# Optimization experiments

Measured on AMD Instinct MI355X. Metric: run time of the kernel, lower is better.

The kernel has to match this reference:

```python
import jax, jax.numpy as jnp
import numpy as np

EPS_LN = 1e-5
EPS_COS = 1e-8
EPS_AREA = 5e-4


def _ln(x, g, b):
    m = jnp.mean(x, axis=-1, keepdims=True)
    v = jnp.mean((x - m) ** 2, axis=-1, keepdims=True)
    return (x - m) / jnp.sqrt(v + EPS_LN) * g + b


def _wgap(f, m):
    # f: (b, N, c), m: (b, N) -> (b, c); matches masked avg_pool2d trick
    num = jnp.einsum('bnc,bn->bc', f, m)
    den = jnp.sum(m, axis=1, keepdims=True) + EPS_AREA
    return num / den


def _cos_tok(k, p):
    # k: (b, N, c) tokens vs p: (b, c) prototype, cosine over channel dim
    dot = jnp.einsum('bnc,bc->bn', k, p)
    nk = jnp.linalg.norm(k, axis=-1)
    np_ = jnp.linalg.norm(p, axis=-1, keepdims=True)
    return dot / (jnp.maximum(nk, EPS_COS) * jnp.maximum(np_, EPS_COS))


def _cos_vec(a, b):
    # a, b: (b, c) -> (b,)
    dot = jnp.sum(a * b, axis=-1)
    na = jnp.linalg.norm(a, axis=-1)
    nb = jnp.linalg.norm(b, axis=-1)
    return dot / (jnp.maximum(na, EPS_COS) * jnp.maximum(nb, EPS_COS))


def _mlp(x, W1, b1, W2, b2):
    h = jax.nn.gelu(x @ W1.T + b1, approximate=False)
    return h @ W2.T + b2


def setup_inputs() -> dict:
    key = jax.random.key(0)
    ks = jax.random.split(key, 32)
    b, H, W, c = 8, 64, 64, 512
    N = H * W
    hid = 4 * c
    s = 0.02
    inp = {
        'x': jax.random.normal(ks[0], (b, N, c), jnp.float32),
        'y': jax.random.normal(ks[1], (b, N, c), jnp.float32),
        'mask': (jax.random.uniform(ks[2], (b, N)) > 0.5).astype(jnp.float32),
        'pro_pred': jax.random.uniform(ks[3], (b, 1, H, W), jnp.float32),
        'g1': jnp.ones((c,), jnp.float32), 'beta1': jnp.zeros((c,), jnp.float32),
        'g2': jnp.ones((c,), jnp.float32), 'beta2': jnp.zeros((c,), jnp.float32),
        'Wq': jax.random.normal(ks[4], (c, c)) * s,
        'Wk': jax.random.normal(ks[5], (c, c)) * s,
        'Wv': jax.random.normal(ks[6], (c, c)) * s,
        'Wx1': jax.random.normal(ks[7], (c, 2 * c)) * s,
        'Wx2': jax.random.normal(ks[8], (c, 2 * c)) * s,
        'Wfx': jax.random.normal(ks[9], (c, 2 * c)) * s,
        'Wy1': jax.random.normal(ks[10], (c, 2 * c)) * s,
        'Wy2': jax.random.normal(ks[11], (c, 2 * c)) * s,
        'Wfy': jax.random.normal(ks[12], (c, 2 * c)) * s,
        'W1x': jax.random.normal(ks[13], (hid, c)) * s, 'b1x': jnp.zeros((hid,)),
        'W2x': jax.random.normal(ks[14], (c, hid)) * s, 'b2x': jnp.zeros((c,)),
        'W1y': jax.random.normal(ks[15], (hid, c)) * s, 'b1y': jnp.zeros((hid,)),
        'W2y': jax.random.normal(ks[16], (c, hid)) * s, 'b2y': jnp.zeros((c,)),
        'h': 64, 'w': 64,
    }
    return inp


def reference(x, y, mask, pro_pred, g1, beta1, g2, beta2, Wq, Wk, Wv,
              Wx1, Wx2, Wfx, Wy1, Wy2, Wfy,
              W1x, b1x, W2x, b2x, W1y, b1y, W2y, b2y, h, w):
    b, N, c = x.shape
    x_skip, y_skip = x, y
    xn = _ln(x, g1, beta1)
    yn = _ln(y, g1, beta1)
    q = yn @ Wq.T            # support features (b, N, c)
    k = xn @ Wk.T            # query features
    v = xn @ Wv.T

    m = mask                 # (b, N)
    fg_pro = _wgap(q, m)             # (b, c)
    bg_pro = _wgap(q, 1.0 - m)

    sim_fg = _cos_tok(k, fg_pro) * 10.0   # (b, N)
    sim_bg = _cos_tok(k, bg_pro) * 10.0
    logits = jnp.stack([sim_bg, sim_fg], axis=1)     # (b, 2, N)
    pseudo = jax.nn.softmax(logits, axis=1)

    query_fg1 = _wgap(v, pseudo[:, 1, :])            # (b, c)
    s1 = (_cos_vec(query_fg1, fg_pro)[:, None] + 1.0) / 2.0
    pro1 = s1 * fg_pro + (1.0 - s1) * query_fg1      # (b, c)

    query_fg2 = _wgap(v, pro_pred.reshape(b, N))
    s2 = (_cos_vec(query_fg2, fg_pro)[:, None] + 1.0) / 2.0
    pro2 = s2 * fg_pro + (1.0 - s2) * query_fg2

    p1 = jnp.broadcast_to(pro1[:, None, :], (b, N, c))
    p2 = jnp.broadcast_to(pro2[:, None, :], (b, N, c))

    x1 = jnp.concatenate([x_skip, p1], axis=-1) @ Wx1.T
    x2 = jnp.concatenate([x_skip, p2], axis=-1) @ Wx2.T
    x_merge = jnp.concatenate([x1, x2], axis=-1) @ Wfx.T + x_skip

    y1 = jnp.concatenate([y_skip, p1], axis=-1) @ Wy1.T
    y2 = jnp.concatenate([y_skip, p2], axis=-1) @ Wy2.T
    y_merge = jnp.concatenate([y1, y2], axis=-1) @ Wfy.T + y_skip

    x_out = x + _mlp(_ln(x_merge, g2, beta2), W1x, b1x, W2x, b2x)
    y_out = y + _mlp(_ln(y_merge, g2, beta2), W1y, b1y, W2y, b2y)
    pseudo_mask = pseudo.reshape(b, 2, h, w)
    return x_out, y_out, pseudo_mask
```

## Files before the change

kernel.cpp:

```cpp
#include <hip/hip_runtime.h>
#include <stdint.h>

typedef unsigned short u16;
typedef unsigned int   u32;

typedef __attribute__((ext_vector_type(8))) __bf16 bf16x8;
typedef __attribute__((ext_vector_type(4))) float  f32x4;

#define GLD_LDS(g, l) __builtin_amdgcn_global_load_lds( \
    (__attribute__((address_space(1))) void*)(g),        \
    (__attribute__((address_space(3))) void*)(l), 16, 0, 0)

__device__ __forceinline__ float bf2f(u16 h) {
    union { u32 u; float f; } c; c.u = ((u32)h) << 16; return c.f;
}
__device__ __forceinline__ u16 f2bf(float f) {
    union { float f; u32 u; } c; c.f = f;
    return (u16)((c.u + 0x7FFFu + ((c.u >> 16) & 1u)) >> 16);
}
__device__ __forceinline__ u32 pack2(float a, float b) {
    return (u32)f2bf(a) | ((u32)f2bf(b) << 16);
}
__device__ __forceinline__ uint4 pack8(float4 a, float4 b) {
    return make_uint4(pack2(a.x, a.y), pack2(a.z, a.w), pack2(b.x, b.y), pack2(b.z, b.w));
}
__device__ __forceinline__ void unpack8(uint4 u, float v[8]) {
    v[0] = bf2f((u16)(u.x & 0xffff)); v[1] = bf2f((u16)(u.x >> 16));
    v[2] = bf2f((u16)(u.y & 0xffff)); v[3] = bf2f((u16)(u.y >> 16));
    v[4] = bf2f((u16)(u.z & 0xffff)); v[5] = bf2f((u16)(u.z >> 16));
    v[6] = bf2f((u16)(u.w & 0xffff)); v[7] = bf2f((u16)(u.w >> 16));
}
__device__ __forceinline__ float wsum(float v) {
#pragma unroll
    for (int o = 32; o > 0; o >>= 1) v += __shfl_xor(v, o, 64);
    return v;
}
__device__ __forceinline__ float fast_gelu(float x) {
    const float u = x * (1.f + 0.044715f * x * x);
    return x / (1.f + __expf(-1.5957691216f * u));
}

__global__ __launch_bounds__(256)
void cvt4_kernel(const float* __restrict__ a, const float* __restrict__ b,
                 const float* __restrict__ c, const float* __restrict__ d,
                 u16* __restrict__ oa, u16* __restrict__ ob,
                 u16* __restrict__ oc, u16* __restrict__ od, int n8)
{
    const int i = blockIdx.x * 256 + threadIdx.x;
    if (i >= n8) return;
    const int z = blockIdx.y;
    const float* in = (z == 0) ? a : (z == 1) ? b : (z == 2) ? c : d;
    u16* out = (z == 0) ? oa : (z == 1) ? ob : (z == 2) ? oc : od;
    const float* p = in + (size_t)i * 8;
    float4 u = *(const float4*)p, v = *(const float4*)(p + 4);
    *(uint4*)(out + (size_t)i * 8) = pack8(u, v);
}
__global__ __launch_bounds__(256)
void cvt3_kernel(const float* __restrict__ a, const float* __restrict__ b,
                 const float* __restrict__ c,
                 u16* __restrict__ oa, u16* __restrict__ ob, u16* __restrict__ oc, int n8)
{
    const int i = blockIdx.x * 256 + threadIdx.x;
    if (i >= n8) return;
    const int z = blockIdx.y;
    const float* in = (z == 0) ? a : (z == 1) ? b : c;
    u16* out = (z == 0) ? oa : (z == 1) ? ob : oc;
    const float* p = in + (size_t)i * 8;
    float4 u = *(const float4*)p, v = *(const float4*)(p + 4);
    *(uint4*)(out + (size_t)i * 8) = pack8(u, v);
}

template<bool IN16, bool RAW>
__device__ __forceinline__ void ln_body(const void* in, u16* out,
                                        const float* g, const float* be, u16* raw_out)
{
    const int lane = threadIdx.x & 63;
    const size_t row = (size_t)blockIdx.x * 4 + (threadIdx.x >> 6);
    const size_t base = row * 512 + lane * 8;
    float v[8];
    if constexpr (IN16) {
        unpack8(*(const uint4*)((const u16*)in + base), v);
    } else {
        const float* p = (const float*)in + base;
        float4 a = *(const float4*)p, b = *(const float4*)(p + 4);
        v[0]=a.x; v[1]=a.y; v[2]=a.z; v[3]=a.w; v[4]=b.x; v[5]=b.y; v[6]=b.z; v[7]=b.w;
    }
    if constexpr (RAW) {
        u32 ro[4];
#pragma unroll
        for (int i = 0; i < 4; ++i) ro[i] = pack2(v[2*i], v[2*i+1]);
        *(uint4*)(raw_out + base) = make_uint4(ro[0], ro[1], ro[2], ro[3]);
    }
    float s = 0.f, ss = 0.f;
#pragma unroll
    for (int i = 0; i < 8; ++i) { s += v[i]; ss += v[i] * v[i]; }
    s = wsum(s); ss = wsum(ss);
    const float mean = s * (1.f / 512.f);
    const float rstd = rsqrtf(ss * (1.f / 512.f) - mean * mean + 1e-5f);
    const float* gp = g + lane * 8;
    const float* bp = be + lane * 8;
    u32 o[4];
#pragma unroll
    for (int i = 0; i < 4; ++i) {
        u16 lo = f2bf((v[2*i]   - mean) * rstd * gp[2*i]   + bp[2*i]);
        u16 hi = f2bf((v[2*i+1] - mean) * rstd * gp[2*i+1] + bp[2*i+1]);
        o[i] = (u32)lo | ((u32)hi << 16);
    }
    *(uint4*)(out + base) = make_uint4(o[0], o[1], o[2], o[3]);
}

template<bool IN16, bool RAW>
__global__ __launch_bounds__(256)
void ln_kernel(const void* __restrict__ in, u16* __restrict__ out,
               const float* __restrict__ g, const float* __restrict__ be,
               u16* __restrict__ raw_out)
{
    ln_body<IN16, RAW>(in, out, g, be, raw_out);
}

template<bool IN16, bool RAW>
__global__ __launch_bounds__(256)
void ln2_kernel(const void* __restrict__ in0, u16* __restrict__ out0, u16* __restrict__ raw0,
                const void* __restrict__ in1, u16* __restrict__ out1, u16* __restrict__ raw1,
                const float* __restrict__ g, const float* __restrict__ be)
{
    if (blockIdx.y == 0) ln_body<IN16, RAW>(in0, out0, g, be, raw0);
    else                 ln_body<IN16, RAW>(in1, out1, g, be, raw1);
}

template<bool IS16>
__device__ __forceinline__ void load_pair(const void* P, size_t off, size_t rstep,
                                          uint4& r0, uint4& r1)
{
    if constexpr (IS16) {
        const u16* p = (const u16*)P + off;
        r0 = *(const uint4*)p;
        r1 = *(const uint4*)(p + rstep);
    } else {
        const float* p = (const float*)P + off;
        float4 a0 = *(const float4*)p,           a1 = *(const float4*)(p + 4);
        float4 b0 = *(const float4*)(p + rstep), b1 = *(const float4*)(p + rstep + 4);
        r0 = pack8(a0, a1);
        r1 = pack8(b0, b1);
    }
}

template<int EPI, bool OUT16>
__global__ __launch_bounds__(512)
void gemm3_kernel(const u16* __restrict__ A, const u16* __restrict__ B,
                  void* __restrict__ Cp, int N, int K,
                  const float* __restrict__ bias_b,
                  const float* __restrict__ bias_v,
                  const float* __restrict__ skip)
{
    __shared__ u16 sA[2][128 * 32];
    __shared__ u16 sB[2][256 * 32];
    const int t = threadIdx.x;
    const int w = t >> 6;
    const int lane = t & 63;
    const int lr = lane & 15;
    const int lk = lane >> 4;
    const int bm0 = blockIdx.x * 128;
    const int bn0 = blockIdx.y * 256;
    const int wrow = (w >> 2) * 64;
    const int wcol = (w & 3) * 64;

    f32x4 acc[4][4];
#pragma unroll
    for (int m = 0; m < 4; ++m)
#pragma unroll
        for (int n = 0; n < 4; ++n) acc[m][n] = (f32x4){0.f, 0.f, 0.f, 0.f};

    const int scol = ((t & 3) ^ ((t >> 3) & 3)) * 8;
    const u16* gA = A + (size_t)(bm0 + (t >> 2)) * K + scol;
    const u16* gB = B + (size_t)(bn0 + (t >> 2)) * K + scol;
    const size_t rstep = (size_t)128 * K;
    const int wo = w << 9;
    const int sa = (lk ^ ((lr >> 1) & 3)) * 8;

    GLD_LDS(gA, sA[0] + wo);
    GLD_LDS(gB, sB[0] + wo);
    GLD_LDS(gB + rstep, sB[0] + 4096 + wo);
    __syncthreads();

    int cur = 0;
    for (int kt = 32; kt <= K; kt += 32) {
        if (kt < K) {
            const int nxt = cur ^ 1;
            GLD_LDS(gA + kt, sA[nxt] + wo);
            GLD_LDS(gB + kt, sB[nxt] + wo);
            GLD_LDS(gB + kt + rstep, sB[nxt] + 4096 + wo);
        }
        bf16x8 af[4], bfr[4];
#pragma unroll
        for (int m = 0; m < 4; ++m)
            af[m] = *(const bf16x8*)&sA[cur][(wrow + m * 16 + lr) * 32 + sa];
#pragma unroll
        for (int n = 0; n < 4; ++n)
            bfr[n] = *(const bf16x8*)&sB[cur][(wcol + n * 16 + lr) * 32 + sa];
#pragma unroll
        for (int m = 0; m < 4; ++m)
#pragma unroll
            for (int n = 0; n < 4; ++n)
                acc[m][n] = __builtin_amdgcn_mfma_f32_16x16x32_bf16(af[m], bfr[n], acc[m][n], 0, 0, 0);
        if (kt < K) { __syncthreads(); cur ^= 1; }
    }

#pragma unroll
    for (int m = 0; m < 4; ++m) {
#pragma unroll
        for (int n = 0; n < 4; ++n) {
            const int col = bn0 + wcol + n * 16 + lr;
#pragma unroll
            for (int r = 0; r < 4; ++r) {
                const int row = bm0 + wrow + m * 16 + lk * 4 + r;
                const size_t idx = (size_t)row * N + col;
                float vv = acc[m][n][r];
                if (EPI == 1) vv += bias_b[(size_t)(row >> 12) * N + col] + skip[idx];
                if (EPI == 2) { vv += bias_v[col]; vv = fast_gelu(vv); }
                if (EPI == 3) vv += bias_v[col] + skip[idx];
                if (OUT16) ((u16*)Cp)[idx] = f2bf(vv);
                else       ((float*)Cp)[idx] = vv;
            }
        }
    }
}

template<int EPI, bool OUT16>
__global__ __launch_bounds__(256)
void gemm2_kernel(const u16* __restrict__ A, const u16* __restrict__ B,
                  void* __restrict__ Cp, int N, int K,
                  const float* __restrict__ bias_b,
                  const float* __restrict__ bias_v,
                  const float* __restrict__ skip)
{
    __shared__ u16 sA[2][128 * 32];
    __shared__ u16 sB[2][128 * 32];
    const int t = threadIdx.x;
    const int w = t >> 6;
    const int lane = t & 63;
    const int lr = lane & 15;
    const int lk = lane >> 4;
    const int bm0 = blockIdx.x * 128;
    const int bn0 = blockIdx.y * 128;
    const int wrow = (w >> 1) * 64;
    const int wcol = (w & 1) * 64;

    f32x4 acc[4][4];
#pragma unroll
    for (int m = 0; m < 4; ++m)
#pragma unroll
        for (int n = 0; n < 4; ++n) acc[m][n] = (f32x4){0.f, 0.f, 0.f, 0.f};

    const int scol = ((t & 3) ^ ((t >> 3) & 3)) * 8;
    const u16* gA = A + (size_t)(bm0 + (t >> 2)) * K + scol;
    const u16* gB = B + (size_t)(bn0 + (t >> 2)) * K + scol;
    const size_t rstep = (size_t)64 * K;
    const int wo = w << 9;
    const int sa = (lk ^ ((lr >> 1) & 3)) * 8;

    GLD_LDS(gA, sA[0] + wo); GLD_LDS(gA + rstep, sA[0] + wo + 2048);
    GLD_LDS(gB, sB[0] + wo); GLD_LDS(gB + rstep, sB[0] + wo + 2048);
    __syncthreads();

    int cur = 0;
    for (int kt = 32; kt <= K; kt += 32) {
        if (kt < K) {
            const int nxt = cur ^ 1;
            GLD_LDS(gA + kt, sA[nxt] + wo); GLD_LDS(gA + kt + rstep, sA[nxt] + wo + 2048);
            GLD_LDS(gB + kt, sB[nxt] + wo); GLD_LDS(gB + kt + rstep, sB[nxt] + wo + 2048);
        }
        bf16x8 af[4], bfr[4];
#pragma unroll
        for (int m = 0; m < 4; ++m)
            af[m] = *(const bf16x8*)&sA[cur][(wrow + m * 16 + lr) * 32 + sa];
#pragma unroll
        for (int n = 0; n < 4; ++n)
            bfr[n] = *(const bf16x8*)&sB[cur][(wcol + n * 16 + lr) * 32 + sa];
#pragma unroll
        for (int m = 0; m < 4; ++m)
#pragma unroll
            for (int n = 0; n < 4; ++n)
                acc[m][n] = __builtin_amdgcn_mfma_f32_16x16x32_bf16(af[m], bfr[n], acc[m][n], 0, 0, 0);
        if (kt < K) { __syncthreads(); cur ^= 1; }
    }

#pragma unroll
    for (int m = 0; m < 4; ++m) {
#pragma unroll
        for (int n = 0; n < 4; ++n) {
            const int col = bn0 + wcol + n * 16 + lr;
#pragma unroll
            for (int r = 0; r < 4; ++r) {
                const int row = bm0 + wrow + m * 16 + lk * 4 + r;
                const size_t idx = (size_t)row * N + col;
                float vv = acc[m][n][r];
                if (EPI == 1) vv += bias_b[(size_t)(row >> 12) * N + col] + skip[idx];
                if (EPI == 2) { vv += bias_v[col]; vv = fast_gelu(vv); }
                if (EPI == 3) vv += bias_v[col] + skip[idx];
                if (OUT16) ((u16*)Cp)[idx] = f2bf(vv);
                else       ((float*)Cp)[idx] = vv;
            }
        }
    }
}

template<int WM>
__global__ __launch_bounds__(512)
void gemm3_red_kernel(const u16* __restrict__ A, const u16* __restrict__ B, int K,
                      const float* __restrict__ wa, const float* __restrict__ wb,
                      float* __restrict__ acc1, float* __restrict__ acc2)
{
    __shared__ u16 sA[2][128 * 32];
    __shared__ u16 sB[2][256 * 32];
    __shared__ float sred[8][2][64];
    const int t = threadIdx.x;
    const int w = t >> 6;
    const int lane = t & 63;
    const int lr = lane & 15;
    const int lk = lane >> 4;
    const int bm0 = blockIdx.x * 128;
    const int bn0 = blockIdx.y * 256;
    const int wrow = (w >> 2) * 64;
    const int wcol = (w & 3) * 64;

    f32x4 acc[4][4];
#pragma unroll
    for (int m = 0; m < 4; ++m)
#pragma unroll
        for (int n = 0; n < 4; ++n) acc[m][n] = (f32x4){0.f, 0.f, 0.f, 0.f};

    const int scol = ((t & 3) ^ ((t >> 3) & 3)) * 8;
    const u16* gA = A + (size_t)(bm0 + (t >> 2)) * K + scol;
    const u16* gB = B + (size_t)(bn0 + (t >> 2)) * K + scol;
    const size_t rstep = (size_t)128 * K;
    const int wo = w << 9;
    const int sa = (lk ^ ((lr >> 1) & 3)) * 8;

    GLD_LDS(gA, sA[0] + wo);
    GLD_LDS(gB, sB[0] + wo);
    GLD_LDS(gB + rstep, sB[0] + 4096 + wo);
    __syncthreads();

    int cur = 0;
    for (int kt = 32; kt <= K; kt += 32) {
        if (kt < K) {
            const int nxt = cur ^ 1;
            GLD_LDS(gA + kt, sA[nxt] + wo);
            GLD_LDS(gB + kt, sB[nxt] + wo);
            GLD_LDS(gB + kt + rstep, sB[nxt] + 4096 + wo);
        }
        bf16x8 af[4], bfr[4];
#pragma unroll
        for (int m = 0; m < 4; ++m)
            af[m] = *(const bf16x8*)&sA[cur][(wrow + m * 16 + lr) * 32 + sa];
#pragma unroll
        for (int n = 0; n < 4; ++n)
            bfr[n] = *(const bf16x8*)&sB[cur][(wcol + n * 16 + lr) * 32 + sa];
#pragma unroll
        for (int m = 0; m < 4; ++m)
#pragma unroll
            for (int n = 0; n < 4; ++n)
                acc[m][n] = __builtin_amdgcn_mfma_f32_16x16x32_bf16(af[m], bfr[n], acc[m][n], 0, 0, 0);
        if (kt < K) { __syncthreads(); cur ^= 1; }
    }

    float w1v[16], w2v[16];
#pragma unroll
    for (int m = 0; m < 4; ++m)
#pragma unroll
        for (int r = 0; r < 4; ++r) {
            const int row = bm0 + wrow + m * 16 + lk * 4 + r;
            if (WM == 0) { float mm = wa[row]; w1v[m*4+r] = mm; w2v[m*4+r] = 1.f - mm; }
            else         { w1v[m*4+r] = wa[row]; w2v[m*4+r] = wb[row]; }
        }
    __syncthreads();
#pragma unroll
    for (int n = 0; n < 4; ++n) {
        float s1 = 0.f, s2 = 0.f;
#pragma unroll
        for (int m = 0; m < 4; ++m)
#pragma unroll
            for (int r = 0; r < 4; ++r) {
                s1 += acc[m][n][r] * w1v[m*4+r];
                s2 += acc[m][n][r] * w2v[m*4+r];
            }
        s1 += __shfl_xor(s1, 16, 64); s1 += __shfl_xor(s1, 32, 64);
        s2 += __shfl_xor(s2, 16, 64); s2 += __shfl_xor(s2, 32, 64);
        if (lk == 0) { sred[w][0][n*16+lr] = s1; sred[w][1][n*16+lr] = s2; }
    }
    __syncthreads();
    if (t < 256) {
        const int strip = t >> 6, c = t & 63;
        const float v1 = sred[strip][0][c] + sred[strip + 4][0][c];
        const float v2 = sred[strip][1][c] + sred[strip + 4][1][c];
        const int col = bn0 + strip * 64 + c;
        const int b = bm0 >> 12;
        atomicAdd(&acc1[b * 512 + col], v1);
        atomicAdd(&acc2[b * 512 + col], v2);
    }
}

template<int EPI, bool A16, bool B16, bool OUT16>
__global__ __launch_bounds__(256)
void gemm_kernel(const void* __restrict__ Ap, const void* __restrict__ Wp,
                 void* __restrict__ Cp, int N, int K,
                 const float* __restrict__ bias_b,
                 const float* __restrict__ bias_v,
                 const float* __restrict__ skip)
{
    __shared__ u16 sA[128 * 32];
    __shared__ u16 sB[128 * 32];
    const int t = threadIdx.x;
    const int w = t >> 6;
    const int lane = t & 63;
    const int lr = lane & 15;
    const int lk = lane >> 4;
    const int bm0 = blockIdx.x * 128;
    const int bn0 = blockIdx.y * 128;
    const int wrow = (w >> 1) * 64;
    const int wcol = (w & 1) * 64;

    f32x4 acc[4][4];
#pragma unroll
    for (int m = 0; m < 4; ++m)
#pragma unroll
        for (int n = 0; n < 4; ++n) acc[m][n] = (f32x4){0.f, 0.f, 0.f, 0.f};

    const size_t aoff = (size_t)(bm0 + (t >> 2)) * K + (t & 3) * 8;
    const size_t boff = (size_t)(bn0 + (t >> 2)) * K + (t & 3) * 8;
    const size_t rstep = (size_t)64 * K;
    u16* dA = sA + 8 * t;
    u16* dB = sB + 8 * t;

    for (int kt = 0; kt < K; kt += 32) {
        uint4 ra0, ra1, rb0, rb1;
        load_pair<A16>(Ap, aoff + kt, rstep, ra0, ra1);
        load_pair<B16>(Wp, boff + kt, rstep, rb0, rb1);
        __syncthreads();
        *(uint4*)dA = ra0; *(uint4*)(dA + 2048) = ra1;
        *(uint4*)dB = rb0; *(uint4*)(dB + 2048) = rb1;
        __syncthreads();
        bf16x8 af[4], bfr[4];
#pragma unroll
        for (int m = 0; m < 4; ++m)
            af[m] = *(const bf16x8*)&sA[(wrow + m * 16 + lr) * 32 + lk * 8];
#pragma unroll
        for (int n = 0; n < 4; ++n)
            bfr[n] = *(const bf16x8*)&sB[(wcol + n * 16 + lr) * 32 + lk * 8];
#pragma unroll
        for (int m = 0; m < 4; ++m)
#pragma unroll
            for (int n = 0; n < 4; ++n)
                acc[m][n] = __builtin_amdgcn_mfma_f32_16x16x32_bf16(af[m], bfr[n], acc[m][n], 0, 0, 0);
    }

#pragma unroll
    for (int m = 0; m < 4; ++m) {
#pragma unroll
        for (int n = 0; n < 4; ++n) {
            const int col = bn0 + wcol + n * 16 + lr;
#pragma unroll
            for (int r = 0; r < 4; ++r) {
                const int row = bm0 + wrow + m * 16 + lk * 4 + r;
                const size_t idx = (size_t)row * N + col;
                float vv = acc[m][n][r];
                if (EPI == 1) vv += bias_b[(size_t)(row >> 12) * N + col] + skip[idx];
                if (EPI == 2) { vv += bias_v[col]; vv = fast_gelu(vv); }
                if (EPI == 3) vv += bias_v[col] + skip[idx];
                if (OUT16) ((u16*)Cp)[idx] = f2bf(vv);
                else       ((float*)Cp)[idx] = vv;
            }
        }
    }
}

template<int WM>
__global__ __launch_bounds__(256)
void gemm_red_kernel(const u16* __restrict__ A, const float* __restrict__ W, int K,
                     const float* __restrict__ wa, const float* __restrict__ wb,
                     float* __restrict__ acc1, float* __restrict__ acc2)
{
    __shared__ u16 sA[128 * 32];
    __shared__ u16 sB[128 * 32];
    __shared__ float sred[4][2][64];
    const int t = threadIdx.x;
    const int w = t >> 6;
    const int lane = t & 63;
    const int lr = lane & 15;
    const int lk = lane >> 4;
    const int bm0 = blockIdx.x * 128;
    const int bn0 = blockIdx.y * 128;
    const int wrow = (w >> 1) * 64;
    const int wcol = (w & 1) * 64;

    f32x4 acc[4][4];
#pragma unroll
    for (int m = 0; m < 4; ++m)
#pragma unroll
        for (int n = 0; n < 4; ++n) acc[m][n] = (f32x4){0.f, 0.f, 0.f, 0.f};

    const size_t aoff = (size_t)(bm0 + (t >> 2)) * K + (t & 3) * 8;
    const size_t boff = (size_t)(bn0 + (t >> 2)) * K + (t & 3) * 8;
    const size_t rstep = (size_t)64 * K;
    u16* dA = sA + 8 * t;
    u16* dB = sB + 8 * t;

    for (int kt = 0; kt < K; kt += 32) {
        uint4 ra0, ra1, rb0, rb1;
        load_pair<true >(A, aoff + kt, rstep, ra0, ra1);
        load_pair<false>(W, boff + kt, rstep, rb0, rb1);
        __syncthreads();
        *(uint4*)dA = ra0; *(uint4*)(dA + 2048) = ra1;
        *(uint4*)dB = rb0; *(uint4*)(dB + 2048) = rb1;
        __syncthreads();
        bf16x8 af[4], bfr[4];
#pragma unroll
        for (int m = 0; m < 4; ++m)
            af[m] = *(const bf16x8*)&sA[(wrow + m * 16 + lr) * 32 + lk * 8];
#pragma unroll
        for (int n = 0; n < 4; ++n)
            bfr[n] = *(const bf16x8*)&sB[(wcol + n * 16 + lr) * 32 + lk * 8];
#pragma unroll
        for (int m = 0; m < 4; ++m)
#pragma unroll
            for (int n = 0; n < 4; ++n)
                acc[m][n] = __builtin_amdgcn_mfma_f32_16x16x32_bf16(af[m], bfr[n], acc[m][n], 0, 0, 0);
    }

    float w1v[16], w2v[16];
#pragma unroll
    for (int m = 0; m < 4; ++m)
#pragma unroll
        for (int r = 0; r < 4; ++r) {
            const int row = bm0 + wrow + m * 16 + lk * 4 + r;
            if (WM == 0) { float mm = wa[row]; w1v[m*4+r] = mm; w2v[m*4+r] = 1.f - mm; }
            else         { w1v[m*4+r] = wa[row]; w2v[m*4+r] = wb[row]; }
        }
#pragma unroll
    for (int n = 0; n < 4; ++n) {
        float s1 = 0.f, s2 = 0.f;
#pragma unroll
        for (int m = 0; m < 4; ++m)
#pragma unroll
            for (int r = 0; r < 4; ++r) {
                s1 += acc[m][n][r] * w1v[m*4+r];
                s2 += acc[m][n][r] * w2v[m*4+r];
            }
        s1 += __shfl_xor(s1, 16, 64); s1 += __shfl_xor(s1, 32, 64);
        s2 += __shfl_xor(s2, 16, 64); s2 += __shfl_xor(s2, 32, 64);
        if (lk == 0) { sred[w][0][n*16+lr] = s1; sred[w][1][n*16+lr] = s2; }
    }
    __syncthreads();
// ... 119 lines not shown
                    const float* __restrict__ Wfy, const float* __restrict__ Wy1,
                    const float* __restrict__ Wy2, u16* __restrict__ My)
{
    const float* Wf = blockIdx.z ? Wfy : Wfx;
    const float* W1 = blockIdx.z ? Wy1 : Wx1;
    const float* W2 = blockIdx.z ? Wy2 : Wx2;
    u16* Mout = blockIdx.z ? My : Mx;
    const int i = blockIdx.x * 16 + threadIdx.x;
    const int o = blockIdx.y * 16 + threadIdx.y;
    float s = 0.f;
    for (int j = 0; j < 512; ++j) {
        s += Wf[o * 1024 + j]       * W1[j * 1024 + i];
        s += Wf[o * 1024 + 512 + j] * W2[j * 1024 + i];
    }
    Mout[o * 512 + i] = f2bf(s);
}

__global__ __launch_bounds__(512)
void tvec4_kernel(const float* __restrict__ Wx1, const float* __restrict__ Wx2,
                  const float* __restrict__ Wy1, const float* __restrict__ Wy2,
                  const float* __restrict__ pro1, const float* __restrict__ pro2,
                  float* __restrict__ t1x, float* __restrict__ t2x,
                  float* __restrict__ t1y, float* __restrict__ t2y)
{
    const int z = blockIdx.z;
    const float* W = (z == 0) ? Wx1 : (z == 1) ? Wx2 : (z == 2) ? Wy1 : Wy2;
    const float* p = (z & 1) ? pro2 : pro1;
    float* tout = (z == 0) ? t1x : (z == 1) ? t2x : (z == 2) ? t1y : t2y;
    const int lane = threadIdx.x & 63;
    const int j = blockIdx.x * 8 + (threadIdx.x >> 6);
    const int b = blockIdx.y;
    const float* wr = W + (size_t)j * 1024 + 512 + lane * 8;
    const float* pr = p + b * 512 + lane * 8;
    float4 w0 = *(const float4*)wr, w1 = *(const float4*)(wr + 4);
    float4 p0 = *(const float4*)pr, p1 = *(const float4*)(pr + 4);
    float s = w0.x*p0.x + w0.y*p0.y + w0.z*p0.z + w0.w*p0.w
            + w1.x*p1.x + w1.y*p1.y + w1.z*p1.z + w1.w*p1.w;
    s = wsum(s);
    if (lane == 0) tout[b * 512 + j] = s;
}

__global__ __launch_bounds__(512)
void biascomb2_kernel(const float* __restrict__ Wfx, const float* __restrict__ Wfy,
                      const float* __restrict__ t1x, const float* __restrict__ t2x,
                      const float* __restrict__ t1y, const float* __restrict__ t2y,
                      float* __restrict__ bias_x, float* __restrict__ bias_y)
{
    const int z = blockIdx.z;
    const float* Wf = z ? Wfy : Wfx;
    const float* t1 = z ? t1y : t1x;
    const float* t2 = z ? t2y : t2x;
    float* bias = z ? bias_y : bias_x;
    const int lane = threadIdx.x & 63;
    const int o = blockIdx.x * 8 + (threadIdx.x >> 6);
    const int b = blockIdx.y;
    const float* w1 = Wf + (size_t)o * 1024 + lane * 8;
    const float* tp1 = t1 + b * 512 + lane * 8;
    const float* tp2 = t2 + b * 512 + lane * 8;
    float s = 0.f;
#pragma unroll
    for (int h = 0; h < 2; ++h) {
        const float* wv = w1 + h * 512;
        const float* tp = h ? tp2 : tp1;
        float4 a0 = *(const float4*)wv, a1 = *(const float4*)(wv + 4);
        float4 b0 = *(const float4*)tp, b1 = *(const float4*)(tp + 4);
        s += a0.x*b0.x + a0.y*b0.y + a0.z*b0.z + a0.w*b0.w
           + a1.x*b1.x + a1.y*b1.y + a1.z*b1.z + a1.w*b1.w;
    }
    s = wsum(s);
    if (lane == 0) bias[b * 512 + o] = s;
}

extern "C" void kernel_launch(void* const* d_in, const int* in_sizes, int n_in,
                              void* d_out, int out_size, void* d_ws, size_t ws_size,
                              hipStream_t stream)
{
    const float* x   = (const float*)d_in[0];
    const float* y   = (const float*)d_in[1];
    const float* mask= (const float*)d_in[2];
    const float* pp  = (const float*)d_in[3];
    const float* g1  = (const float*)d_in[4];
    const float* be1 = (const float*)d_in[5];
    const float* g2  = (const float*)d_in[6];
    const float* be2 = (const float*)d_in[7];
    const float* Wq  = (const float*)d_in[8];
    const float* Wk  = (const float*)d_in[9];
    const float* Wv  = (const float*)d_in[10];
    const float* Wx1 = (const float*)d_in[11];
    const float* Wx2 = (const float*)d_in[12];
    const float* Wfx = (const float*)d_in[13];
    const float* Wy1 = (const float*)d_in[14];
    const float* Wy2 = (const float*)d_in[15];
    const float* Wfy = (const float*)d_in[16];
    const float* W1x = (const float*)d_in[17];
    const float* b1x = (const float*)d_in[18];
    const float* W2x = (const float*)d_in[19];
    const float* b2x = (const float*)d_in[20];
    const float* W1y = (const float*)d_in[21];
    const float* b1y = (const float*)d_in[22];
    const float* W2y = (const float*)d_in[23];
    const float* b2y = (const float*)d_in[24];

    if (ws_size < 69206016u) return;
    const bool fast = ws_size >= 78643200u;
    const bool huge = ws_size >= 145752064u;

    float* outx = (float*)d_out;
    float* outy = outx + 16777216;
    float* pmf  = outx + 33554432;

    char* wsb = (char*)d_ws;
    float* fsm = (float*)wsb;
    float* fgacc  = fsm;
    float* bgacc  = fsm + 4096;
    float* q1acc  = fsm + 8192;
    float* q2acc  = fsm + 12288;
    float* denq1  = fsm + 16384;
    float* denfg  = fsm + 16392;
    float* denq2  = fsm + 16400;
    float* nfg    = fsm + 16408;
    float* nbg    = fsm + 16416;
    float* fg_pro = fsm + 16424;
    float* bg_pro = fsm + 20520;
    float* pro1   = fsm + 24616;
    float* pro2   = fsm + 28712;
    float* t1x    = fsm + 32808;
    float* t2x    = fsm + 36904;
    float* t1y    = fsm + 41000;
    float* t2y    = fsm + 45096;
    float* bias_x = fsm + 49192;
    float* bias_y = fsm + 53288;
    float* pseudo = fsm + 57384;

    hipMemsetAsync(fsm, 0, 65568, stream);

    if (fast) {
        u16* Mx   = (u16*)(wsb + 0x60000);
        u16* My   = (u16*)(wsb + 0xE0000);
        u16* Wqb  = (u16*)(wsb + 0x160000);
        u16* Wkb  = (u16*)(wsb + 0x1E0000);
        u16* Wvb  = (u16*)(wsb + 0x260000);
        u16* W1xb = (u16*)(wsb + 0x2E0000);
        u16* W2xb = (u16*)(wsb + 0x4E0000);
        u16* W1yb = (u16*)(wsb + 0x6E0000);
        u16* W2yb = (u16*)(wsb + 0x8E0000);
        u16* WS0  = (u16*)(wsb + 0xB00000);
        u16* WS1  = WS0 + 16777216;
        u16* WS2  = WS1 + 16777216;

        u16* OX0 = (u16*)outx;
        u16* OX1 = OX0 + 16777216;
        u16* OY  = (u16*)outy;

        cvt3_kernel<<<dim3(128, 3), 256, 0, stream>>>(Wq, Wk, Wv, Wqb, Wkb, Wvb, 32768);
        cvt4_kernel<<<dim3(512, 4), 256, 0, stream>>>(W1x, W2x, W1y, W2y, W1xb, W2xb, W1yb, W2yb, 131072);
        mmcomb2_kernel<<<dim3(32, 32, 2), dim3(16, 16), 0, stream>>>(Wfx, Wx1, Wx2, Mx, Wfy, Wy1, Wy2, My);

        ln2_kernel<false, true><<<dim3(8192, 2), 256, 0, stream>>>(x, WS0, OX0, y, WS1, OY, g1, be1);

        dim3 gq(256, 2);
        gemm3_red_kernel<0><<<gq, 512, 0, stream>>>(WS1, Wqb, 512, mask, nullptr, fgacc, bgacc);
        rowsum2_kernel<<<dim3(8, 2), 256, 0, stream>>>(mask, denfg, pp, denq2);
        proto_fin_kernel<<<8, 512, 0, stream>>>(fgacc, bgacc, denfg, fg_pro, bg_pro, nfg, nbg);

        gemm3_kernel<0, true><<<gq, 512, 0, stream>>>(WS0, Wkb, OX1, 512, 512, nullptr, nullptr, nullptr);
        sim_kernel<<<8192, 256, 0, stream>>>(OX1, fg_pro, bg_pro, nfg, nbg, pseudo, pmf);
        rowsum_kernel<<<8, 256, 0, stream>>>(pseudo, denq1);

        gemm3_red_kernel<1><<<gq, 512, 0, stream>>>(WS0, Wvb, 512, pseudo, pp, q1acc, q2acc);
        proto2_kernel<<<8, 512, 0, stream>>>(q1acc, q2acc, denq1, denq2, fg_pro, nfg, pro1, pro2);

        tvec4_kernel<<<dim3(64, 8, 4), 512, 0, stream>>>(Wx1, Wx2, Wy1, Wy2, pro1, pro2, t1x, t2x, t1y, t2y);
        biascomb2_kernel<<<dim3(64, 8, 2), 512, 0, stream>>>(Wfx, Wfy, t1x, t2x, t1y, t2y, bias_x, bias_y);

        gemm3_kernel<1, true><<<gq, 512, 0, stream>>>(OX0, Mx, WS0, 512, 512, bias_x, nullptr, x);
        ln_kernel<true, false><<<8192, 256, 0, stream>>>(WS0, WS1, g2, be2, nullptr);
        gemm3_kernel<1, true><<<gq, 512, 0, stream>>>(OY, My, WS0, 512, 512, bias_y, nullptr, y);
        ln_kernel<true, false><<<8192, 256, 0, stream>>>(WS0, WS0, g2, be2, nullptr);

        for (int ch = 0; ch < 2; ++ch) {
            const size_t ro = (size_t)ch * 16384 * 512;
            gemm3_kernel<2, true><<<dim3(128, 8), 512, 0, stream>>>(WS1 + ro, W1xb, OY, 2048, 512, nullptr, b1x, nullptr);
            gemm2_kernel<3, false><<<dim3(128, 4), 256, 0, stream>>>(OY, W2xb, outx + ro, 512, 2048, nullptr, b2x, x + ro);
        }

        if (huge) {
            for (int ch = 0; ch < 2; ++ch) {
                const size_t ro = (size_t)ch * 16384 * 512;
                gemm3_kernel<2, true><<<dim3(128, 8), 512, 0, stream>>>(WS0 + ro, W1yb, WS2, 2048, 512, nullptr, b1y, nullptr);
                gemm2_kernel<3, false><<<dim3(128, 4), 256, 0, stream>>>(WS2, W2yb, outy + ro, 512, 2048, nullptr, b2y, y + ro);
            }
        } else {
            for (int ch = 0; ch < 4; ++ch) {
                const size_t ro = (size_t)ch * 8192 * 512;
                gemm3_kernel<2, true><<<dim3(64, 8), 512, 0, stream>>>(WS0 + ro, W1yb, WS1, 2048, 512, nullptr, b1y, nullptr);
                gemm2_kernel<3, false><<<dim3(64, 4), 256, 0, stream>>>(WS1, W2yb, outy + ro, 512, 2048, nullptr, b2y, y + ro);
            }
        }
    } else {
        u16* Mx  = (u16*)(wsb + 360608);
        u16* My  = (u16*)(wsb + 884896);
        u16* WS0 = (u16*)(wsb + 2097152);
        u16* WS1 = (u16*)(wsb + 35651584);

        ln_kernel<false, false><<<8192, 256, 0, stream>>>(x, WS0, g1, be1, nullptr);
        ln_kernel<false, false><<<8192, 256, 0, stream>>>(y, WS1, g1, be1, nullptr);

        dim3 g512(256, 4);
        gemm_red_kernel<0><<<g512, 256, 0, stream>>>(WS1, Wq, 512, mask, nullptr, fgacc, bgacc);
        rowsum_kernel<<<8, 256, 0, stream>>>(mask, denfg);
        rowsum_kernel<<<8, 256, 0, stream>>>(pp, denq2);
        proto_fin_kernel<<<8, 512, 0, stream>>>(fgacc, bgacc, denfg, fg_pro, bg_pro, nfg, nbg);

        gemm_kernel<0, true, false, true><<<g512, 256, 0, stream>>>(WS0, Wk, WS1, 512, 512, nullptr, nullptr, nullptr);
        sim_kernel<<<8192, 256, 0, stream>>>(WS1, fg_pro, bg_pro, nfg, nbg, pseudo, pmf);
        rowsum_kernel<<<8, 256, 0, stream>>>(pseudo, denq1);

        gemm_red_kernel<1><<<g512, 256, 0, stream>>>(WS0, Wv, 512, pseudo, pp, q1acc, q2acc);
        proto2_kernel<<<8, 512, 0, stream>>>(q1acc, q2acc, denq1, denq2, fg_pro, nfg, pro1, pro2);

        mmcomb2_kernel<<<dim3(32, 32, 2), dim3(16, 16), 0, stream>>>(Wfx, Wx1, Wx2, Mx, Wfy, Wy1, Wy2, My);
        tvec4_kernel<<<dim3(64, 8, 4), 512, 0, stream>>>(Wx1, Wx2, Wy1, Wy2, pro1, pro2, t1x, t2x, t1y, t2y);
        biascomb2_kernel<<<dim3(64, 8, 2), 512, 0, stream>>>(Wfx, Wfy, t1x, t2x, t1y, t2y, bias_x, bias_y);

        gemm_kernel<1, false, true, true><<<g512, 256, 0, stream>>>(x, Mx, WS0, 512, 512, bias_x, nullptr, x);
        ln_kernel<true, false><<<8192, 256, 0, stream>>>(WS0, WS1, g2, be2, nullptr);
        for (int ch = 0; ch < 4; ++ch) {
            const size_t ro = (size_t)ch * 8192 * 512;
            gemm_kernel<2, true, false, true><<<dim3(64, 16), 256, 0, stream>>>(WS1 + ro, W1x, WS0, 2048, 512, nullptr, b1x, nullptr);
            gemm_kernel<3, true, false, false><<<dim3(64, 4), 256, 0, stream>>>(WS0, W2x, outx + ro, 512, 2048, nullptr, b2x, x + ro);
        }
        gemm_kernel<1, false, true, true><<<g512, 256, 0, stream>>>(y, My, WS0, 512, 512, bias_y, nullptr, y);
        ln_kernel<true, false><<<8192, 256, 0, stream>>>(WS0, WS1, g2, be2, nullptr);
        for (int ch = 0; ch < 4; ++ch) {
            const size_t ro = (size_t)ch * 8192 * 512;
            gemm_kernel<2, true, false, true><<<dim3(64, 16), 256, 0, stream>>>(WS1 + ro, W1y, WS0, 2048, 512, nullptr, b1y, nullptr);
            gemm_kernel<3, true, false, false><<<dim3(64, 4), 256, 0, stream>>>(WS0, W2y, outy + ro, 512, 2048, nullptr, b2y, y + ro);
        }
    }
    (void)in_sizes; (void)n_in; (void)out_size;
}
```

Measured before the change: 871.4 us.

## Batch independent GEMMs into z-indexed launches and compute weight combos with MFMA

Refactors the GEMM kernels into device bodies so that independent GEMMs (the Q-reduction with the K projection, and the x/y merge GEMMs) run as a single launch using blockIdx.z. The per-stream fused merge weight product is now computed by converting and transposing the weights to bf16 and running the MFMA gemm2 path, replacing the previous mmcomb2 kernel. This cuts launch count and gives each launch a larger grid to fill the GPU. In exchange the combined weight matrix is computed in bf16 rather than fp32, and extra conversion and transpose kernels are added.

```diff
diff --git a/kernel.cpp b/kernel.cpp
--- a/kernel.cpp
+++ b/kernel.cpp
@@ -68,6 +68,37 @@
     const float* p = in + (size_t)i * 8;
     float4 u = *(const float4*)p, v = *(const float4*)(p + 4);
     *(uint4*)(out + (size_t)i * 8) = pack8(u, v);
+}
+__global__ __launch_bounds__(256)
+void cvt2_kernel(const float* __restrict__ a, const float* __restrict__ b,
+                 u16* __restrict__ oa, u16* __restrict__ ob, int n8)
+{
+    const int i = blockIdx.x * 256 + threadIdx.x;
+    if (i >= n8) return;
+    const float* in = blockIdx.y ? b : a;
+    u16* out = blockIdx.y ? ob : oa;
+    const float* p = in + (size_t)i * 8;
+    float4 u = *(const float4*)p, v = *(const float4*)(p + 4);
+    *(uint4*)(out + (size_t)i * 8) = pack8(u, v);
+}
+
+__global__ __launch_bounds__(256)
+void wtrans_kernel(const float* __restrict__ W1x, const float* __restrict__ W2x,
+                   const float* __restrict__ W1y, const float* __restrict__ W2y,
+                   u16* __restrict__ Wtx, u16* __restrict__ Wty)
+{
+    __shared__ float tile[32][33];
+    const int z = blockIdx.z;
+    const float* src = (z == 0) ? W1x : (z == 1) ? W2x : (z == 2) ? W1y : W2y;
+    u16* dst = (z < 2) ? Wtx : Wty;
+    const int joff = (z & 1) * 512;
+    const int j0 = blockIdx.y * 32;
+    const int i0 = blockIdx.x * 32;
+    for (int r = threadIdx.y; r < 32; r += 8)
+        tile[r][threadIdx.x] = src[(size_t)(j0 + r) * 1024 + i0 + threadIdx.x];
+    __syncthreads();
+    for (int r = threadIdx.y; r < 32; r += 8)
+        dst[(size_t)(i0 + r) * 1024 + joff + j0 + threadIdx.x] = f2bf(tile[threadIdx.x][r]);
 }
 
 template<bool IN16, bool RAW>
@@ -146,15 +177,10 @@
 }
 
 template<int EPI, bool OUT16>
-__global__ __launch_bounds__(512)
-void gemm3_kernel(const u16* __restrict__ A, const u16* __restrict__ B,
-                  void* __restrict__ Cp, int N, int K,
-                  const float* __restrict__ bias_b,
-                  const float* __restrict__ bias_v,
-                  const float* __restrict__ skip)
-{
-    __shared__ u16 sA[2][128 * 32];
-    __shared__ u16 sB[2][256 * 32];
+__device__ __forceinline__ void gemm3_body(const u16* A, const u16* B, void* Cp, int N, int K,
+                                           const float* bias_b, const float* bias_v, const float* skip,
+                                           u16 sA[2][128 * 32], u16 sB[2][256 * 32])
+{
     const int t = threadIdx.x;
     const int w = t >> 6;
     const int lane = t & 63;
@@ -226,16 +252,159 @@
     }
 }
 
+template<int WM>
+__device__ __forceinline__ void gemm3red_body(const u16* A, const u16* B, int K,
+                                              const float* wa, const float* wb,
+                                              float* acc1, float* acc2,
+                                              u16 sA[2][128 * 32], u16 sB[2][256 * 32],
+                                              float sred[8][2][64])
+{
+    const int t = threadIdx.x;
+    const int w = t >> 6;
+    const int lane = t & 63;
+    const int lr = lane & 15;
+    const int lk = lane >> 4;
+    const int bm0 = blockIdx.x * 128;
+    const int bn0 = blockIdx.y * 256;
+    const int wrow = (w >> 2) * 64;
+    const int wcol = (w & 3) * 64;
+
+    f32x4 acc[4][4];
+#pragma unroll
+    for (int m = 0; m < 4; ++m)
+#pragma unroll
+        for (int n = 0; n < 4; ++n) acc[m][n] = (f32x4){0.f, 0.f, 0.f, 0.f};
+
+    const int scol = ((t & 3) ^ ((t >> 3) & 3)) * 8;
+    const u16* gA = A + (size_t)(bm0 + (t >> 2)) * K + scol;
+    const u16* gB = B + (size_t)(bn0 + (t >> 2)) * K + scol;
+    const size_t rstep = (size_t)128 * K;
+    const int wo = w << 9;
+    const int sa = (lk ^ ((lr >> 1) & 3)) * 8;
+
+    GLD_LDS(gA, sA[0] + wo);
+    GLD_LDS(gB, sB[0] + wo);
+    GLD_LDS(gB + rstep, sB[0] + 4096 + wo);
+    __syncthreads();
+
+    int cur = 0;
+    for (int kt = 32; kt <= K; kt += 32) {
+        if (kt < K) {
+            const int nxt = cur ^ 1;
+            GLD_LDS(gA + kt, sA[nxt] + wo);
+            GLD_LDS(gB + kt, sB[nxt] + wo);
+            GLD_LDS(gB + kt + rstep, sB[nxt] + 4096 + wo);
+        }
+        bf16x8 af[4], bfr[4];
+#pragma unroll
+        for (int m = 0; m < 4; ++m)
+            af[m] = *(const bf16x8*)&sA[cur][(wrow + m * 16 + lr) * 32 + sa];
+#pragma unroll
+        for (int n = 0; n < 4; ++n)
+            bfr[n] = *(const bf16x8*)&sB[cur][(wcol + n * 16 + lr) * 32 + sa];
+#pragma unroll
+        for (int m = 0; m < 4; ++m)
+#pragma unroll
+            for (int n = 0; n < 4; ++n)
+                acc[m][n] = __builtin_amdgcn_mfma_f32_16x16x32_bf16(af[m], bfr[n], acc[m][n], 0, 0, 0);
+        if (kt < K) { __syncthreads(); cur ^= 1; }
+    }
+
+    float w1v[16], w2v[16];
+#pragma unroll
+    for (int m = 0; m < 4; ++m)
+#pragma unroll
+        for (int r = 0; r < 4; ++r) {
+            const int row = bm0 + wrow + m * 16 + lk * 4 + r;
+            if (WM == 0) { float mm = wa[row]; w1v[m*4+r] = mm; w2v[m*4+r] = 1.f - mm; }
+            else         { w1v[m*4+r] = wa[row]; w2v[m*4+r] = wb[row]; }
+        }
+    __syncthreads();
+#pragma unroll
+    for (int n = 0; n < 4; ++n) {
+        float s1 = 0.f, s2 = 0.f;
+#pragma unroll
+        for (int m = 0; m < 4; ++m)
+#pragma unroll
+            for (int r = 0; r < 4; ++r) {
+                s1 += acc[m][n][r] * w1v[m*4+r];
+                s2 += acc[m][n][r] * w2v[m*4+r];
+            }
+        s1 += __shfl_xor(s1, 16, 64); s1 += __shfl_xor(s1, 32, 64);
+        s2 += __shfl_xor(s2, 16, 64); s2 += __shfl_xor(s2, 32, 64);
+        if (lk == 0) { sred[w][0][n*16+lr] = s1; sred[w][1][n*16+lr] = s2; }
+    }
+    __syncthreads();
+    if (t < 256) {
+        const int strip = t >> 6, c = t & 63;
+        const float v1 = sred[strip][0][c] + sred[strip + 4][0][c];
+        const float v2 = sred[strip][1][c] + sred[strip + 4][1][c];
+        const int col = bn0 + strip * 64 + c;
+        const int b = bm0 >> 12;
+        atomicAdd(&acc1[b * 512 + col], v1);
+        atomicAdd(&acc2[b * 512 + col], v2);
+    }
+}
+
 template<int EPI, bool OUT16>
-__global__ __launch_bounds__(256)
-void gemm2_kernel(const u16* __restrict__ A, const u16* __restrict__ B,
+__global__ __launch_bounds__(512)
+void gemm3_kernel(const u16* __restrict__ A, const u16* __restrict__ B,
                   void* __restrict__ Cp, int N, int K,
                   const float* __restrict__ bias_b,
                   const float* __restrict__ bias_v,
                   const float* __restrict__ skip)
 {
     __shared__ u16 sA[2][128 * 32];
-    __shared__ u16 sB[2][128 * 32];
+    __shared__ u16 sB[2][256 * 32];
+    gemm3_body<EPI, OUT16>(A, B, Cp, N, K, bias_b, bias_v, skip, sA, sB);
+}
+
+template<int WM>
+__global__ __launch_bounds__(512)
+void gemm3_red_kernel(const u16* __restrict__ A, const u16* __restrict__ B, int K,
+                      const float* __restrict__ wa, const float* __restrict__ wb,
+                      float* __restrict__ acc1, float* __restrict__ acc2)
+{
+    __shared__ u16 sA[2][128 * 32];
+    __shared__ u16 sB[2][256 * 32];
+    __shared__ float sred[8][2][64];
+    gemm3red_body<WM>(A, B, K, wa, wb, acc1, acc2, sA, sB, sred);
+}
+
+__global__ __launch_bounds__(512)
+void qk_mix_kernel(const u16* __restrict__ Ayn, const u16* __restrict__ Wqb,
+                   const float* __restrict__ mask, float* __restrict__ fgacc, float* __restrict__ bgacc,
+                   const u16* __restrict__ Axn, const u16* __restrict__ Wkb, u16* __restrict__ Ck,
+                   int N, int K)
+{
+    __shared__ u16 sA[2][128 * 32];
+    __shared__ u16 sB[2][256 * 32];
+    __shared__ float sred[8][2][64];
+    if (blockIdx.z == 0)
+        gemm3red_body<0>(Ayn, Wqb, K, mask, nullptr, fgacc, bgacc, sA, sB, sred);
+    else
+        gemm3_body<0, true>(Axn, Wkb, Ck, N, K, nullptr, nullptr, nullptr, sA, sB);
+}
+
+template<int EPI, bool OUT16>
+__global__ __launch_bounds__(512)
+void gemm3z_kernel(const u16* __restrict__ A0, const u16* __restrict__ B0, void* __restrict__ C0,
+                   const float* __restrict__ bb0, const float* __restrict__ bv0, const float* __restrict__ sk0,
+                   const u16* __restrict__ A1, const u16* __restrict__ B1, void* __restrict__ C1,
+                   const float* __restrict__ bb1, const float* __restrict__ bv1, const float* __restrict__ sk1,
+                   int N, int K)
+{
+    __shared__ u16 sA[2][128 * 32];
+    __shared__ u16 sB[2][256 * 32];
+    if (blockIdx.z == 0) gemm3_body<EPI, OUT16>(A0, B0, C0, N, K, bb0, bv0, sk0, sA, sB);
+    else                 gemm3_body<EPI, OUT16>(A1, B1, C1, N, K, bb1, bv1, sk1, sA, sB);
+}
+
+template<int EPI, bool OUT16>
+__device__ __forceinline__ void gemm2_body(const u16* A, const u16* B, void* Cp, int N, int K,
+                                           const float* bias_v, const float* skip,
+                                           u16 sA[2][128 * 32], u16 sB[2][128 * 32])
+{
     const int t = threadIdx.x;
     const int w = t >> 6;
     const int lane = t & 63;
@@ -295,7 +464,6 @@
                 const int row = bm0 + wrow + m * 16 + lk * 4 + r;
                 const size_t idx = (size_t)row * N + col;
                 float vv = acc[m][n][r];
-                if (EPI == 1) vv += bias_b[(size_t)(row >> 12) * N + col] + skip[idx];
                 if (EPI == 2) { vv += bias_v[col]; vv = fast_gelu(vv); }
                 if (EPI == 3) vv += bias_v[col] + skip[idx];
                 if (OUT16) ((u16*)Cp)[idx] = f2bf(vv);
@@ -305,100 +473,32 @@
     }
 }
 
-template<int WM>
-__global__ __launch_bounds__(512)
-void gemm3_red_kernel(const u16* __restrict__ A, const u16* __restrict__ B, int K,
-                      const float* __restrict__ wa, const float* __restrict__ wb,
-                      float* __restrict__ acc1, float* __restrict__ acc2)
+template<int EPI, bool OUT16>
+__global__ __launch_bounds__(256)
+void gemm2_kernel(const u16* __restrict__ A, const u16* __restrict__ B,
+                  void* __restrict__ Cp, int N, int K,
+                  const float* __restrict__ bias_b,
+                  const float* __restrict__ bias_v,
+                  const float* __restrict__ skip)
 {
     __shared__ u16 sA[2][128 * 32];
-    __shared__ u16 sB[2][256 * 32];
-    __shared__ float sred[8][2][64];
-    const int t = threadIdx.x;
-    const int w = t >> 6;
-    const int lane = t & 63;
-    const int lr = lane & 15;
-    const int lk = lane >> 4;
-    const int bm0 = blockIdx.x * 128;
-    const int bn0 = blockIdx.y * 256;
-    const int wrow = (w >> 2) * 64;
-    const int wcol = (w & 3) * 64;
-
-    f32x4 acc[4][4];
-#pragma unroll
-    for (int m = 0; m < 4; ++m)
-#pragma unroll
-        for (int n = 0; n < 4; ++n) acc[m][n] = (f32x4){0.f, 0.f, 0.f, 0.f};
-
-    const int scol = ((t & 3) ^ ((t >> 3) & 3)) * 8;
-    const u16* gA = A + (size_t)(bm0 + (t >> 2)) * K + scol;
-    const u16* gB = B + (size_t)(bn0 + (t >> 2)) * K + scol;
-    const size_t rstep = (size_t)128 * K;
-    const int wo = w << 9;
-    const int sa = (lk ^ ((lr >> 1) & 3)) * 8;
-
-    GLD_LDS(gA, sA[0] + wo);
-    GLD_LDS(gB, sB[0] + wo);
-    GLD_LDS(gB + rstep, sB[0] + 4096 + wo);
-    __syncthreads();
-
-    int cur = 0;
-    for (int kt = 32; kt <= K; kt += 32) {
-        if (kt < K) {
-            const int nxt = cur ^ 1;
-            GLD_LDS(gA + kt, sA[nxt] + wo);
-            GLD_LDS(gB + kt, sB[nxt] + wo);
-            GLD_LDS(gB + kt + rstep, sB[nxt] + 4096 + wo);
-        }
-        bf16x8 af[4], bfr[4];
-#pragma unroll
-        for (int m = 0; m < 4; ++m)
-            af[m] = *(const bf16x8*)&sA[cur][(wrow + m * 16 + lr) * 32 + sa];
-#pragma unroll
-        for (int n = 0; n < 4; ++n)
-            bfr[n] = *(const bf16x8*)&sB[cur][(wcol + n * 16 + lr) * 32 + sa];
-#pragma unroll
-        for (int m = 0; m < 4; ++m)
-#pragma unroll
-            for (int n = 0; n < 4; ++n)
-                acc[m][n] = __builtin_amdgcn_mfma_f32_16x16x32_bf16(af[m], bfr[n], acc[m][n], 0, 0, 0);
-        if (kt < K) { __syncthreads(); cur ^= 1; }
-    }
-
-    float w1v[16], w2v[16];
-#pragma unroll
-    for (int m = 0; m < 4; ++m)
-#pragma unroll
-        for (int r = 0; r < 4; ++r) {
-            const int row = bm0 + wrow + m * 16 + lk * 4 + r;
-            if (WM == 0) { float mm = wa[row]; w1v[m*4+r] = mm; w2v[m*4+r] = 1.f - mm; }
-            else         { w1v[m*4+r] = wa[row]; w2v[m*4+r] = wb[row]; }
-        }
-    __syncthreads();
-#pragma unroll
-    for (int n = 0; n < 4; ++n) {
-        float s1 = 0.f, s2 = 0.f;
-#pragma unroll
-        for (int m = 0; m < 4; ++m)
-#pragma unroll
-            for (int r = 0; r < 4; ++r) {
-                s1 += acc[m][n][r] * w1v[m*4+r];
-                s2 += acc[m][n][r] * w2v[m*4+r];
-            }
-        s1 += __shfl_xor(s1, 16, 64); s1 += __shfl_xor(s1, 32, 64);
-        s2 += __shfl_xor(s2, 16, 64); s2 += __shfl_xor(s2, 32, 64);
-        if (lk == 0) { sred[w][0][n*16+lr] = s1; sred[w][1][n*16+lr] = s2; }
-    }
-    __syncthreads();
-    if (t < 256) {
-        const int strip = t >> 6, c = t & 63;
-        const float v1 = sred[strip][0][c] + sred[strip + 4][0][c];
-        const float v2 = sred[strip][1][c] + sred[strip + 4][1][c];
-        const int col = bn0 + strip * 64 + c;
-        const int b = bm0 >> 12;
-        atomicAdd(&acc1[b * 512 + col], v1);
-        atomicAdd(&acc2[b * 512 + col], v2);
-    }
+    __shared__ u16 sB[2][128 * 32];
+    gemm2_body<EPI, OUT16>(A, B, Cp, N, K, bias_v, skip, sA, sB);
+    (void)bias_b;
+}
+
+template<int EPI, bool OUT16>
+__global__ __launch_bounds__(256)
+void gemm2z_kernel(const u16* __restrict__ A0, const u16* __restrict__ B0, void* __restrict__ C0,
+                   const float* __restrict__ bv0, const float* __restrict__ sk0,
+                   const u16* __restrict__ A1, const u16* __restrict__ B1, void* __restrict__ C1,
+                   const float* __restrict__ bv1, const float* __restrict__ sk1,
+                   int N, int K)
+{
+    __shared__ u16 sA[2][128 * 32];
+    __shared__ u16 sB[2][128 * 32];
+    if (blockIdx.z == 0) gemm2_body<EPI, OUT16>(A0, B0, C0, N, K, bv0, sk0, sA, sB);
+    else                 gemm2_body<EPI, OUT16>(A1, B1, C1, N, K, bv1, sk1, sA, sB);
 }
 
 template<int EPI, bool A16, bool B16, bool OUT16>
@@ -824,31 +924,43 @@
         u16* OX1 = OX0 + 16777216;
         u16* OY  = (u16*)outy;
 
+        u16* Wfxb = WS0;
+        u16* Wfyb = WS0 + 524288;
+        u16* Wtx  = WS0 + 1048576;
+        u16* Wty  = WS0 + 1572864;
+
         cvt3_kernel<<<dim3(128, 3), 256, 0, stream>>>(Wq, Wk, Wv, Wqb, Wkb, Wvb, 32768);
         cvt4_kernel<<<dim3(512, 4), 256, 0, stream>>>(W1x, W2x, W1y, W2y, W1xb, W2xb, W1yb, W2yb, 131072);
-        mmcomb2_kernel<<<dim3(32, 32, 2), dim3(16, 16), 0, stream>>>(Wfx, Wx1, Wx2, Mx, Wfy, Wy1, Wy2, My);
+        cvt2_kernel<<<dim3(256, 2), 256, 0, stream>>>(Wfx, Wfy, Wfxb, Wfyb, 65536);
+        wtrans_kernel<<<dim3(16, 16, 4), dim3(32, 8), 0, stream>>>(Wx1, Wx2, Wy1, Wy2, Wtx, Wty);
+        gemm2z_kernel<0, true><<<dim3(4, 4, 2), 256, 0, stream>>>(
+            Wfxb, Wtx, Mx, nullptr, nullptr,
+            Wfyb, Wty, My, nullptr, nullptr, 512, 1024);
 
         ln2_kernel<false, true><<<dim3(8192, 2), 256, 0, stream>>>(x, WS0, OX0, y, WS1, OY, g1, be1);
 
-        dim3 gq(256, 2);
-        gemm3_red_kernel<0><<<gq, 512, 0, stream>>>(WS1, Wqb, 512, mask, nullptr, fgacc, bgacc);
         rowsum2_kernel<<<dim3(8, 2), 256, 0, stream>>>(mask, denfg, pp, denq2);
+
+        qk_mix_kernel<<<dim3(256, 2, 2), 512, 0, stream>>>(
+            WS1, Wqb, mask, fgacc, bgacc,
+            WS0, Wkb, OX1, 512, 512);
+
         proto_fin_kernel<<<8, 512, 0, stream>>>(fgacc, bgacc, denfg, fg_pro, bg_pro, nfg, nbg);
-
-        gemm3_kernel<0, true><<<gq, 512, 0, stream>>>(WS0, Wkb, OX1, 512, 512, nullptr, nullptr, nullptr);
         sim_kernel<<<8192, 256, 0, stream>>>(OX1, fg_pro, bg_pro, nfg, nbg, pseudo, pmf);
         rowsum_kernel<<<8, 256, 0, stream>>>(pseudo, denq1);
 
-        gemm3_red_kernel<1><<<gq, 512, 0, stream>>>(WS0, Wvb, 512, pseudo, pp, q1acc, q2acc);
+        gemm3_red_kernel<1><<<dim3(256, 2), 512, 0, stream>>>(WS0, Wvb, 512, pseudo, pp, q1acc, q2acc);
         proto2_kernel<<<8, 512, 0, stream>>>(q1acc, q2acc, denq1, denq2, fg_pro, nfg, pro1, pro2);
 
         tvec4_kernel<<<dim3(64, 8, 4), 512, 0, stream>>>(Wx1, Wx2, Wy1, Wy2, pro1, pro2, t1x, t2x, t1y, t2y);
         biascomb2_kernel<<<dim3(64, 8, 2), 512, 0, stream>>>(Wfx, Wfy, t1x, t2x, t1y, t2y, bias_x, bias_y);
 
-        gemm3_kernel<1, true><<<gq, 512, 0, stream>>>(OX0, Mx, WS0, 512, 512, bias_x, nullptr, x);
+        gemm3z_kernel<1, true><<<dim3(256, 2, 2), 512, 0, stream>>>(
+            OX0, Mx, WS0, bias_x, nullptr, x,
+            OY,  My, OX1, bias_y, nullptr, y, 512, 512);
+
         ln_kernel<true, false><<<8192, 256, 0, stream>>>(WS0, WS1, g2, be2, nullptr);
-        gemm3_kernel<1, true><<<gq, 512, 0, stream>>>(OY, My, WS0, 512, 512, bias_y, nullptr, y);
-        ln_kernel<true, false><<<8192, 256, 0, stream>>>(WS0, WS0, g2, be2, nullptr);
+        ln_kernel<true, false><<<8192, 256, 0, stream>>>(OX1, WS0, g2, be2, nullptr);
 
         for (int ch = 0; ch < 2; ++ch) {
             const size_t ro = (size_t)ch * 16384 * 512;
```

New measurement: 772.5 us. 11.4% less time.
